# Kernel tuning notes

Measured on AMD Instinct MI355X. Metric: run time of the kernel, lower is better.

Reference implementation:

```python
import jax, jax.numpy as jnp
import numpy as np

B, N, C = 4, 4096, 1024
NUM_HEADS = 16
HEAD_DIM = C // NUM_HEADS


def setup_inputs() -> dict:
    key = jax.random.key(0)
    k1, k2, k3, k4 = jax.random.split(key, 4)
    s_in = 1.0 / np.sqrt(C)
    return {
        "x": jax.random.normal(k1, (B, N, C), dtype=jnp.float32),
        "H": 64,
        "W": 64,
        "Wqkv": jax.random.normal(k2, (3 * C, C), dtype=jnp.float32) * s_in,
        "Wproj": jax.random.normal(k3, (C, C), dtype=jnp.float32) * s_in,
        "bproj": jnp.zeros((C,), dtype=jnp.float32),
        "alpha": jnp.ones((NUM_HEADS,), dtype=jnp.float32),
    }


def reference(x, H, W, Wqkv, Wproj, bproj, alpha):
    Bb, Nn, Cc = x.shape
    h, d = NUM_HEADS, HEAD_DIM
    # qkv: [B, N, 3C] -> [3, B, h, N, d]
    qkv = jnp.einsum('bnc,oc->bno', x, Wqkv)
    qkv = qkv.reshape(Bb, Nn, 3, h, d).transpose(2, 0, 3, 1, 4)
    q, k, v = qkv[0], qkv[1], qkv[2]  # each [B, h, N, d]
    # channel attention: contract over tokens N -> [B, h, d, d]
    attn = jnp.einsum('bhnd,bhne->bhde', k, q) / alpha[None, :, None, None]
    attn = jax.nn.softmax(attn, axis=-1)
    # (dropout is identity in eval/reference mode)
    # head_out: [B, h, d, N] -> transpose -> [B, N, h, d] -> concat heads
    out = jnp.einsum('bhde,bhne->bhdn', attn, v)
    out = out.transpose(0, 3, 1, 2).reshape(Bb, Nn, Cc)
    return jnp.einsum('bnc,oc->bno', out, Wproj) + bproj
```

## Files before the change

kernel.cpp:

```cpp
#include <hip/hip_runtime.h>
#include <hip/hip_bf16.h>
#include <cstdint>
#include <cstddef>

typedef unsigned short u16;
typedef __bf16 bf16x8 __attribute__((ext_vector_type(8)));
typedef float f32x4 __attribute__((ext_vector_type(4)));
typedef unsigned short u16x4 __attribute__((ext_vector_type(4)));
typedef unsigned short u16x8 __attribute__((ext_vector_type(8)));

#define AS1(p) ((__attribute__((address_space(1))) void*)(p))
#define AS3(p) ((__attribute__((address_space(3))) void*)(p))

__device__ __forceinline__ float bf2f(u16 u) {
  unsigned v = ((unsigned)u) << 16; float f; __builtin_memcpy(&f, &v, 4); return f;
}
__device__ __forceinline__ u16 f2bf(float f) {
  unsigned u; __builtin_memcpy(&u, &f, 4);
  u += 0x7FFFu + ((u >> 16) & 1u);
  return (u16)(u >> 16);
}

__global__ __launch_bounds__(256) void convert_kernel(const float* __restrict__ src,
                                                      u16* __restrict__ dst, int n4) {
// ... 54 lines not shown
      llo[(c4 + i) * 72 + rs] = lo[i];
    }
  }
  __syncthreads();
  const int c  = t >> 2;
  const int n0 = (t & 3) * 16;
  const int rot_r = ((t >> 4) & 3) << 4;
  const int nA = n0 ^ rot_r;
  const size_t tbase = ((size_t)b * 1024 + cT * 64 + c) * 4096 + nT * 64 + n0;
  *(u16x8*)(XThi + tbase)     = *(const u16x8*)(lhi + c * 72 + nA);
  *(u16x8*)(XThi + tbase + 8) = *(const u16x8*)(lhi + c * 72 + nA + 8);
  *(u16x8*)(XTlo + tbase)     = *(const u16x8*)(llo + c * 72 + nA);
  *(u16x8*)(XTlo + tbase + 8) = *(const u16x8*)(llo + c * 72 + nA + 8);
}

template<bool OUT_BF16, bool HAS_BIAS>
__global__ __launch_bounds__(512, 2) void gemm_pipe(const u16* __restrict__ A,
                                                    const u16* __restrict__ B,
                                                    void* __restrict__ Cv,
                                                    const float* __restrict__ bias,
                                                    int M, int N, int K,
                                                    size_t sA, size_t sB, size_t sC) {
  __shared__ __align__(16) u16 lds[4][2][8192];
  const int tid  = threadIdx.x;
  const int lane = tid & 63;
  const int wave = tid >> 6;
  const int wm = wave >> 2, wn = wave & 3;
  const int rowTile = blockIdx.x * 256;
  const int colTile = blockIdx.y * 256;
  A += (size_t)blockIdx.z * sA;
  B += (size_t)blockIdx.z * sB;

  size_t srcA[2], srcB[2];
  int ldsOff[2];
#pragma unroll
  for (int j = 0; j < 2; ++j) {
    const int L = j * 512 + tid;
    const int sr = L >> 3;
    const int slot = (L & 7) ^ (sr & 7);
    const int r  = (sr << 1) | (slot >> 2);
    const int kq = slot & 3;
    srcA[j] = (size_t)(rowTile + r) * K + kq * 8;
    srcB[j] = (size_t)(colTile + r) * K + kq * 8;
    ldsOff[j] = (j * 512 + (tid & 448)) * 16;
  }

  const int m15 = lane & 15, kq4 = lane >> 4;
  const int r0a = wm * 128 + m15, sa0 = r0a >> 1;
  const int idxA0 = sa0 * 64 + (((((r0a & 1) << 2) | kq4)) ^ (sa0 & 7)) * 8;
  const int r0b = wn * 64 + m15, sb0 = r0b >> 1;
  const int idxB0 = sb0 * 64 + (((((r0b & 1) << 2) | kq4)) ^ (sb0 & 7)) * 8;

  const int NT = K >> 5;

  auto stageA = [&](int tt) {
    char* d = (char*)&lds[tt & 3][0][0];
    const int kt = tt << 5;
#pragma unroll
    for (int j = 0; j < 2; ++j)
      __builtin_amdgcn_global_load_lds(AS1(A + srcA[j] + kt), AS3(d + ldsOff[j]), 16, 0, 0);
  };
  auto stageB = [&](int tt) {
    char* d = (char*)&lds[tt & 3][1][0];
    const int kt = tt << 5;
#pragma unroll
    for (int j = 0; j < 2; ++j)
      __builtin_amdgcn_global_load_lds(AS1(B + srcB[j] + kt), AS3(d + ldsOff[j]), 16, 0, 0);
  };

  stageA(0); stageB(0);
  if (NT > 1) { stageA(1); stageB(1); }
  if (NT > 2) { stageA(2); stageB(2); }
  if (NT > 2) asm volatile("s_waitcnt vmcnt(8)" ::: "memory");
  else        asm volatile("s_waitcnt vmcnt(0)" ::: "memory");
  __builtin_amdgcn_sched_barrier(0);
  __builtin_amdgcn_s_barrier();
  __builtin_amdgcn_sched_barrier(0);

  f32x4 acc[8][4] = {};
  for (int t = 0; t < NT; ++t) {
    const u16* bufA = &lds[t & 3][0][0];
    const u16* bufB = &lds[t & 3][1][0];
    bf16x8 a[8], bfr[4];
#pragma unroll
    for (int ni = 0; ni < 4; ++ni) bfr[ni] = *(const bf16x8*)(bufB + idxB0 + ni * 512);
#pragma unroll
    for (int mi = 0; mi < 4; ++mi) a[mi] = *(const bf16x8*)(bufA + idxA0 + mi * 512);
    if (t + 3 < NT) stageA(t + 3);
    __builtin_amdgcn_sched_barrier(0);
    __builtin_amdgcn_s_barrier();
    __builtin_amdgcn_sched_barrier(0);
    __builtin_amdgcn_s_setprio(1);
#pragma unroll
    for (int mi = 0; mi < 4; ++mi)
#pragma unroll
      for (int ni = 0; ni < 4; ++ni)
        acc[mi][ni] = __builtin_amdgcn_mfma_f32_16x16x32_bf16(a[mi], bfr[ni], acc[mi][ni], 0, 0, 0);
    __builtin_amdgcn_s_setprio(0);
    __builtin_amdgcn_sched_barrier(0);
    __builtin_amdgcn_s_barrier();
    __builtin_amdgcn_sched_barrier(0);
#pragma unroll
    for (int mi = 4; mi < 8; ++mi) a[mi] = *(const bf16x8*)(bufA + idxA0 + mi * 512);
    if (t + 3 < NT) stageB(t + 3);
    __builtin_amdgcn_sched_barrier(0);
    __builtin_amdgcn_s_barrier();
    __builtin_amdgcn_sched_barrier(0);
    __builtin_amdgcn_s_setprio(1);
#pragma unroll
    for (int mi = 4; mi < 8; ++mi)
#pragma unroll
      for (int ni = 0; ni < 4; ++ni)
        acc[mi][ni] = __builtin_amdgcn_mfma_f32_16x16x32_bf16(a[mi], bfr[ni], acc[mi][ni], 0, 0, 0);
    __builtin_amdgcn_s_setprio(0);
    if (t < NT - 1) {
      if (t + 3 < NT)      asm volatile("s_waitcnt vmcnt(8)" ::: "memory");
      else if (t + 2 < NT) asm volatile("s_waitcnt vmcnt(4)" ::: "memory");
      else                 asm volatile("s_waitcnt vmcnt(0)" ::: "memory");
    }
    __builtin_amdgcn_sched_barrier(0);
    __builtin_amdgcn_s_barrier();
    __builtin_amdgcn_sched_barrier(0);
  }

  const int crow0 = rowTile + wm * 128 + (lane >> 4) * 4;
  const int ccol0 = colTile + wn * 64 + m15;
  if constexpr (OUT_BF16) {
    u16* C = (u16*)Cv + (size_t)blockIdx.z * sC;
#pragma unroll
    for (int mi = 0; mi < 8; ++mi)
#pragma unroll
      for (int ni = 0; ni < 4; ++ni) {
        const int col = ccol0 + ni * 16;
        const float bv = HAS_BIAS ? bias[col] : 0.f;
#pragma unroll
        for (int r = 0; r < 4; ++r)
          C[(size_t)(crow0 + mi * 16 + r) * N + col] = f2bf(acc[mi][ni][r] + bv);
      }
  } else {
    float* C = (float*)Cv + (size_t)blockIdx.z * sC;
#pragma unroll
    for (int mi = 0; mi < 8; ++mi)
#pragma unroll
      for (int ni = 0; ni < 4; ++ni) {
        const int col = ccol0 + ni * 16;
        const float bv = HAS_BIAS ? bias[col] : 0.f;
#pragma unroll
        for (int r = 0; r < 4; ++r)
          C[(size_t)(crow0 + mi * 16 + r) * N + col] = acc[mi][ni][r] + bv;
      }
  }
}

template<int L>
__device__ __forceinline__ void pipe4_core(const u16* __restrict__ pAh,
                                           const u16* __restrict__ pAl,
                                           const u16* __restrict__ pBh,
                                           const u16* __restrict__ pBl,
                                           u16* lds, int ldsByteOff,
                                           int idxA0, int idxB0, int bOff, int NT,
                                           f32x4 acc[4][2]) {
  auto stage2A = [&](int tt) {
    u16* d = lds + (tt & 3) * 16384;
    const int kt = tt << 5;
    __builtin_amdgcn_global_load_lds(AS1(pAh + kt), AS3((char*)d + ldsByteOff), 16, 0, 0);
    __builtin_amdgcn_global_load_lds(AS1(pAl + kt), AS3((char*)(d + 4096) + ldsByteOff), 16, 0, 0);
  };
  auto stage2B = [&](int tt) {
    if constexpr (L == 4) {
      u16* d = lds + (tt & 3) * 16384 + 8192;
      const int kt = tt << 5;
      __builtin_amdgcn_global_load_lds(AS1(pBh + kt), AS3((char*)d + ldsByteOff), 16, 0, 0);
      __builtin_amdgcn_global_load_lds(AS1(pBl + kt), AS3((char*)(d + 4096) + ldsByteOff), 16, 0, 0);
    }
  };

  stage2A(0); stage2B(0);
  stage2A(1); stage2B(1);
  stage2A(2); stage2B(2);
  if constexpr (L == 4) asm volatile("s_waitcnt vmcnt(8)" ::: "memory");
  else                  asm volatile("s_waitcnt vmcnt(4)" ::: "memory");
  __builtin_amdgcn_sched_barrier(0);
  __builtin_amdgcn_s_barrier();
  __builtin_amdgcn_sched_barrier(0);

  for (int t = 0; t < NT; ++t) {
    const u16* base = lds + (t & 3) * 16384;
    bf16x8 ah[4], al[4], bh[2], bl[2];
    bh[0] = *(const bf16x8*)(base + bOff + idxB0);
    bh[1] = *(const bf16x8*)(base + bOff + idxB0 + 512);
    bl[0] = *(const bf16x8*)(base + bOff + 4096 + idxB0);
    bl[1] = *(const bf16x8*)(base + bOff + 4096 + idxB0 + 512);
    ah[0] = *(const bf16x8*)(base + idxA0);
    ah[1] = *(const bf16x8*)(base + idxA0 + 512);
    al[0] = *(const bf16x8*)(base + 4096 + idxA0);
    al[1] = *(const bf16x8*)(base + 4096 + idxA0 + 512);
    if (t + 3 < NT) stage2A(t + 3);
    __builtin_amdgcn_sched_barrier(0);
    __builtin_amdgcn_s_barrier();
    __builtin_amdgcn_sched_barrier(0);
    __builtin_amdgcn_s_setprio(1);
#pragma unroll
    for (int mi = 0; mi < 2; ++mi)
#pragma unroll
      for (int ni = 0; ni < 2; ++ni) {
        acc[mi][ni] = __builtin_amdgcn_mfma_f32_16x16x32_bf16(ah[mi], bh[ni], acc[mi][ni], 0, 0, 0);
        acc[mi][ni] = __builtin_amdgcn_mfma_f32_16x16x32_bf16(ah[mi], bl[ni], acc[mi][ni], 0, 0, 0);
        acc[mi][ni] = __builtin_amdgcn_mfma_f32_16x16x32_bf16(al[mi], bh[ni], acc[mi][ni], 0, 0, 0);
      }
    __builtin_amdgcn_s_setprio(0);
    __builtin_amdgcn_sched_barrier(0);
    __builtin_amdgcn_s_barrier();
    __builtin_amdgcn_sched_barrier(0);
    ah[2] = *(const bf16x8*)(base + idxA0 + 1024);
    ah[3] = *(const bf16x8*)(base + idxA0 + 1536);
    al[2] = *(const bf16x8*)(base + 4096 + idxA0 + 1024);
    al[3] = *(const bf16x8*)(base + 4096 + idxA0 + 1536);
    if (t + 3 < NT) stage2B(t + 3);
    __builtin_amdgcn_sched_barrier(0);
    __builtin_amdgcn_s_barrier();
    __builtin_amdgcn_sched_barrier(0);
    __builtin_amdgcn_s_setprio(1);
#pragma unroll
    for (int mi = 2; mi < 4; ++mi)
#pragma unroll
      for (int ni = 0; ni < 2; ++ni) {
        acc[mi][ni] = __builtin_amdgcn_mfma_f32_16x16x32_bf16(ah[mi], bh[ni], acc[mi][ni], 0, 0, 0);
        acc[mi][ni] = __builtin_amdgcn_mfma_f32_16x16x32_bf16(ah[mi], bl[ni], acc[mi][ni], 0, 0, 0);
        acc[mi][ni] = __builtin_amdgcn_mfma_f32_16x16x32_bf16(al[mi], bh[ni], acc[mi][ni], 0, 0, 0);
      }
    __builtin_amdgcn_s_setprio(0);
    if (t < NT - 1) {
      if constexpr (L == 4) {
        if (t + 3 < NT)      asm volatile("s_waitcnt vmcnt(8)" ::: "memory");
        else if (t + 2 < NT) asm volatile("s_waitcnt vmcnt(4)" ::: "memory");
        else                 asm volatile("s_waitcnt vmcnt(0)" ::: "memory");
      } else {
        if (t + 3 < NT)      asm volatile("s_waitcnt vmcnt(4)" ::: "memory");
        else if (t + 2 < NT) asm volatile("s_waitcnt vmcnt(2)" ::: "memory");
        else                 asm volatile("s_waitcnt vmcnt(0)" ::: "memory");
      }
    }
    __builtin_amdgcn_sched_barrier(0);
    __builtin_amdgcn_s_barrier();
    __builtin_amdgcn_sched_barrier(0);
  }
}

__global__ __launch_bounds__(512, 2) void gram_pipe(const u16* __restrict__ XThi,
                                                    const u16* __restrict__ XTlo,
                                                    float* __restrict__ Gpart) {
  __shared__ __align__(16) u16 lds[4 * 4 * 4096];
  const int tid = threadIdx.x, lane = tid & 63, wave = tid >> 6;
  const int wm = wave >> 2, wn = wave & 3;
  const int bid = blockIdx.x;
  int b, rT, cT, slice, k0, NT; bool same = false;
  if (bid < 64) {
    b = bid & 3; const int j2 = bid >> 2;
    rT = cT = j2 >> 1; slice = j2 & 1; k0 = slice * 2048; NT = 64; same = true;
  } else {
    const int q = bid - 64;
    const int band = q / 112;
    const int e = q % 112;
    b = e & 3; const int pr = e >> 2;
    int t = pr, rt = 0;
    while (t >= 7 - rt) { t -= 7 - rt; ++rt; }
    const int ct = rt + 1 + t;
    constexpr int K0s[4] = {0, 2048, 3584, 3840};
    constexpr int NTs[4] = {64, 48, 8, 8};
    k0 = K0s[band]; NT = NTs[band]; slice = band & 1;
    if (band < 2) { rT = rt; cT = ct; } else { rT = ct; cT = rt; }
  }
  const int rowTile = rT * 128, colTile = cT * 128;
  const u16* Ah = XThi + ((size_t)b << 22);
  const u16* Al = XTlo + ((size_t)b << 22);

  const int sr = tid >> 3;
  const int slot = (tid & 7) ^ (sr & 7);
  const int r = (sr << 1) | (slot >> 2);
  const int kq8 = (slot & 3) * 8;
  const u16* pAh = Ah + (size_t)(rowTile + r) * 4096 + k0 + kq8;
  const u16* pAl = Al + (size_t)(rowTile + r) * 4096 + k0 + kq8;
  const u16* pBh = Ah + (size_t)(colTile + r) * 4096 + k0 + kq8;
  const u16* pBl = Al + (size_t)(colTile + r) * 4096 + k0 + kq8;
  const int ldsByteOff = (tid & 448) * 16;

  const int m15 = lane & 15, kq4 = lane >> 4;
  const int r0a = wm * 64 + m15, sa0 = r0a >> 1;
  const int idxA0 = sa0 * 64 + (((((r0a & 1) << 2) | kq4)) ^ (sa0 & 7)) * 8;
  const int r0b = wn * 32 + m15, sb0 = r0b >> 1;
  const int idxB0 = sb0 * 64 + (((((r0b & 1) << 2) | kq4)) ^ (sb0 & 7)) * 8;

  f32x4 acc[4][2] = {};
  if (same) pipe4_core<2>(pAh, pAl, pAh, pAl, lds, ldsByteOff, idxA0, idxB0, 0, NT, acc);
  else      pipe4_core<4>(pAh, pAl, pBh, pBl, lds, ldsByteOff, idxA0, idxB0, 8192, NT, acc);

  float* out = Gpart + ((size_t)(slice * 4 + b) << 20);
  const int crow0 = rowTile + wm * 64 + (lane >> 4) * 4;
  const int ccol0 = colTile + wn * 32 + m15;
#pragma unroll
  for (int mi = 0; mi < 4; ++mi)
#pragma unroll
    for (int ni = 0; ni < 2; ++ni)
#pragma unroll
      for (int r4 = 0; r4 < 4; ++r4)
        out[(size_t)(crow0 + mi * 16 + r4) * 1024 + ccol0 + ni * 16] = acc[mi][ni][r4];
}

__global__ __launch_bounds__(256) void gram_reduce_split(const float* __restrict__ Gp,
                                                         u16* __restrict__ Ghi,
                                                         u16* __restrict__ Glo) {
  const int rt = blockIdx.x, ct = blockIdx.y, b = blockIdx.z;
  const bool diag128 = (rt >> 1) == (ct >> 1);
  const float* s0 = Gp + ((size_t)b << 20);
  const float* s1 = Gp + ((size_t)(4 + b) << 20);
  __shared__ float lT[64 * 68];
  const int t = threadIdx.x;
  const int r = t >> 2;
  const int c16 = (t & 3) * 16;

  if (!diag128) {
    const size_t bb = (size_t)(ct * 64 + r) * 1024 + rt * 64 + c16;
#pragma unroll
    for (int q = 0; q < 4; ++q) {
      float4 v0 = *(const float4*)(s0 + bb + q * 4);
      float4 v1 = *(const float4*)(s1 + bb + q * 4);
      float4 s = { v0.x + v1.x, v0.y + v1.y, v0.z + v1.z, v0.w + v1.w };
      *(float4*)(lT + r * 68 + c16 + q * 4) = s;
    }
    __syncthreads();
  }

  const size_t ab = (size_t)(rt * 64 + r) * 1024 + ct * 64 + c16;
  const size_t ob = ((size_t)b << 20) + ab;
#pragma unroll
  for (int q = 0; q < 4; ++q) {
    float4 v0 = *(const float4*)(s0 + ab + q * 4);
    float4 v1 = *(const float4*)(s1 + ab + q * 4);
    float g[4] = { v0.x + v1.x, v0.y + v1.y, v0.z + v1.z, v0.w + v1.w };
    if (!diag128) {
#pragma unroll
      for (int i = 0; i < 4; ++i) g[i] += lT[(c16 + q * 4 + i) * 68 + r];
    }
    u16x4 oh, ol;
    oh.x = f2bf(g[0]); ol.x = f2bf(g[0] - bf2f(oh.x));
    oh.y = f2bf(g[1]); ol.y = f2bf(g[1] - bf2f(oh.y));
    oh.z = f2bf(g[2]); ol.z = f2bf(g[2] - bf2f(oh.z));
    oh.w = f2bf(g[3]); ol.w = f2bf(g[3] - bf2f(oh.w));
    *(u16x4*)(Ghi + ob + q * 4) = oh;
    *(u16x4*)(Glo + ob + q * 4) = ol;
  }
}

__global__ __launch_bounds__(512, 2) void tprime_pipe(const u16* __restrict__ Wqh,
                                                      const u16* __restrict__ Wql,
                                                      const u16* __restrict__ Ghi,
                                                      const u16* __restrict__ Glo,
                                                      u16* __restrict__ Tph,
                                                      u16* __restrict__ Tpl) {
  __shared__ __align__(16) u16 lds[4 * 4 * 4096];
  const int tid = threadIdx.x, lane = tid & 63, wave = tid >> 6;
  const int wm = wave >> 2, wn = wave & 3;
  const int bid = blockIdx.x;
  const int b = bid & 3, tile = bid >> 2;
  const int rowTile = (tile >> 3) * 128, colTile = (tile & 7) * 128;
  const size_t zoff = (size_t)b << 20;

  const int sr = tid >> 3;
  const int slot = (tid & 7) ^ (sr & 7);
  const int r = (sr << 1) | (slot >> 2);
  const int kq8 = (slot & 3) * 8;
  const u16* pAh = Wqh + (size_t)(rowTile + r) * 1024 + kq8;
  const u16* pAl = Wql + (size_t)(rowTile + r) * 1024 + kq8;
  const u16* pBh = Ghi + zoff + (size_t)(colTile + r) * 1024 + kq8;
  const u16* pBl = Glo + zoff + (size_t)(colTile + r) * 1024 + kq8;
  const int ldsByteOff = (tid & 448) * 16;

  const int m15 = lane & 15, kq4 = lane >> 4;
  const int r0a = wm * 64 + m15, sa0 = r0a >> 1;
  const int idxA0 = sa0 * 64 + (((((r0a & 1) << 2) | kq4)) ^ (sa0 & 7)) * 8;
  const int r0b = wn * 32 + m15, sb0 = r0b >> 1;
  const int idxB0 = sb0 * 64 + (((((r0b & 1) << 2) | kq4)) ^ (sb0 & 7)) * 8;

  f32x4 acc[4][2] = {};
  pipe4_core<4>(pAh, pAl, pBh, pBl, lds, ldsByteOff, idxA0, idxB0, 8192, 32, acc);

  const int crow0 = rowTile + wm * 64 + (lane >> 4) * 4;
  const int ccol0 = colTile + wn * 32 + m15;
#pragma unroll
  for (int mi = 0; mi < 4; ++mi)
#pragma unroll
    for (int ni = 0; ni < 2; ++ni)
#pragma unroll
      for (int r4 = 0; r4 < 4; ++r4) {
        float v = acc[mi][ni][r4];
        u16 hi = f2bf(v);
        u16 lo = f2bf(v - bf2f(hi));
        size_t off = zoff + (size_t)(crow0 + mi * 16 + r4) * 1024 + ccol0 + ni * 16;
        Tph[off] = hi;
        Tpl[off] = lo;
      }
}

__global__ __launch_bounds__(256) void s_softmax_kernel(const u16* __restrict__ Wqh,
                                                        const u16* __restrict__ Wql,
                                                        const u16* __restrict__ Tph,
                                                        const u16* __restrict__ Tpl,
                                                        const float* __restrict__ alpha,
                                                        u16* __restrict__ attnT) {
  const int h = blockIdx.x, b = blockIdx.y;
  const int tid = threadIdx.x, lane = tid & 63, wave = tid >> 6;
  __shared__ __align__(16) u16 lAh[64 * 32];
  __shared__ __align__(16) u16 lAl[64 * 32];
  __shared__ __align__(16) u16 lBh[64 * 32];
  __shared__ __align__(16) u16 lBl[64 * 32];

  const size_t aBase = (size_t)(1024 + h * 64) * 1024;
  const size_t bBase = ((size_t)b << 20) + (size_t)(h * 64) * 1024;

  f32x4 acc[4] = {};
  const int m  = lane & 15;
  const int ko = (lane >> 4) * 8;
  const int srow = tid >> 2;
  const int skc  = (tid & 3) * 8;
  const int ldsOff = (tid & 192) * 16;

  for (int kt = 0; kt < 1024; kt += 32) {
    __builtin_amdgcn_global_load_lds(AS1(Wqh + aBase + (size_t)srow * 1024 + kt + skc),
                                     AS3((char*)lAh + ldsOff), 16, 0, 0);
    __builtin_amdgcn_global_load_lds(AS1(Wql + aBase + (size_t)srow * 1024 + kt + skc),
                                     AS3((char*)lAl + ldsOff), 16, 0, 0);
    __builtin_amdgcn_global_load_lds(AS1(Tph + bBase + (size_t)srow * 1024 + kt + skc),
                                     AS3((char*)lBh + ldsOff), 16, 0, 0);
    __builtin_amdgcn_global_load_lds(AS1(Tpl + bBase + (size_t)srow * 1024 + kt + skc),
                                     AS3((char*)lBl + ldsOff), 16, 0, 0);
    __syncthreads();
    bf16x8 ah = *(const bf16x8*)(lAh + (wave * 16 + m) * 32 + ko);
    bf16x8 al = *(const bf16x8*)(lAl + (wave * 16 + m) * 32 + ko);
#pragma unroll
    for (int cb = 0; cb < 4; ++cb) {
      bf16x8 bh = *(const bf16x8*)(lBh + (cb * 16 + m) * 32 + ko);
      bf16x8 bl = *(const bf16x8*)(lBl + (cb * 16 + m) * 32 + ko);
      acc[cb] = __builtin_amdgcn_mfma_f32_16x16x32_bf16(ah, bh, acc[cb], 0, 0, 0);
      acc[cb] = __builtin_amdgcn_mfma_f32_16x16x32_bf16(ah, bl, acc[cb], 0, 0, 0);
      acc[cb] = __builtin_amdgcn_mfma_f32_16x16x32_bf16(al, bh, acc[cb], 0, 0, 0);
    }
    __syncthreads();
  }

  const float invA = 1.f / alpha[h];
  const int g = lane >> 4;
  const size_t obase = (size_t)(b * 16 + h) * 4096;
#pragma unroll
  for (int r = 0; r < 4; ++r) {
    int d = wave * 16 + g * 4 + r;
    float s[4];
#pragma unroll
    for (int cb = 0; cb < 4; ++cb) s[cb] = acc[cb][r] * invA;
    float mx = fmaxf(fmaxf(s[0], s[1]), fmaxf(s[2], s[3]));
#pragma unroll
    for (int o = 1; o < 16; o <<= 1) mx = fmaxf(mx, __shfl_xor(mx, o, 64));
    float e[4]; float sum = 0.f;
#pragma unroll
    for (int cb = 0; cb < 4; ++cb) { e[cb] = __expf(s[cb] - mx); sum += e[cb]; }
#pragma unroll
    for (int o = 1; o < 16; o <<= 1) sum += __shfl_xor(sum, o, 64);
    float inv = 1.f / sum;
#pragma unroll
    for (int cb = 0; cb < 4; ++cb) {
      int e_idx = cb * 16 + (lane & 15);
      attnT[obase + (size_t)e_idx * 64 + d] = f2bf(e[cb] * inv);
    }
  }
}

__global__ __launch_bounds__(256) void m_build_kernel(const u16* __restrict__ Wpb,
                                                      const u16* __restrict__ attnT,
                                                      u16* __restrict__ Mb) {
  const int oT = blockIdx.x, h = blockIdx.y, b = blockIdx.z;
  const int tid = threadIdx.x, lane = tid & 63, wave = tid >> 6;
  __shared__ __align__(16) u16 lA[128 * 64];
  __shared__ __align__(16) u16 lB[64 * 64];
  const int bh = b * 16 + h;
#pragma unroll
  for (int i = 0; i < 4; ++i) {
    int idx = i * 256 + tid;
    int row = idx >> 3;
    int kc  = (idx & 7) * 8;
    int ldsOff = (i * 256 + (tid & 192)) * 16;
    __builtin_amdgcn_global_load_lds(AS1(Wpb + (size_t)(oT * 128 + row) * 1024 + h * 64 + kc),
                                     AS3((char*)lA + ldsOff), 16, 0, 0);
  }
#pragma unroll
  for (int i = 0; i < 2; ++i) {
    int idx = i * 256 + tid;
    int ldsOff = (i * 256 + (tid & 192)) * 16;
    __builtin_amdgcn_global_load_lds(AS1(attnT + (size_t)bh * 4096 + idx * 8),
                                     AS3((char*)lB + ldsOff), 16, 0, 0);
  }
  __syncthreads();
  const int m  = lane & 15;
  const int ko = (lane >> 4) * 8;
  const int wr = wave * 32;
  f32x4 acc[2][4] = {};
#pragma unroll
  for (int ks = 0; ks < 2; ++ks) {
#pragma unroll
    for (int rb = 0; rb < 2; ++rb) {
      bf16x8 a = *(const bf16x8*)(lA + (wr + rb * 16 + m) * 64 + ks * 32 + ko);
#pragma unroll
      for (int cb = 0; cb < 4; ++cb) {
        bf16x8 bb = *(const bf16x8*)(lB + (cb * 16 + m) * 64 + ks * 32 + ko);
        acc[rb][cb] = __builtin_amdgcn_mfma_f32_16x16x32_bf16(a, bb, acc[rb][cb], 0, 0, 0);
      }
    }
  }
  u16* out = Mb + ((size_t)b << 20);
#pragma unroll
  for (int rb = 0; rb < 2; ++rb)
#pragma unroll
    for (int cb = 0; cb < 4; ++cb) {
      int col = h * 64 + cb * 16 + (lane & 15);
#pragma unroll
      for (int r = 0; r < 4; ++r) {
        int row = oT * 128 + wr + rb * 16 + (lane >> 4) * 4 + r;
        out[(size_t)row * 1024 + col] = f2bf(acc[rb][cb][r]);
      }
    }
}

extern "C" void kernel_launch(void* const* d_in, const int* in_sizes, int n_in,
                              void* d_out, int out_size, void* d_ws, size_t ws_size,
                              hipStream_t stream) {
  const float* x     = (const float*)d_in[0];
  const float* Wqkv  = (const float*)d_in[3];
  const float* Wproj = (const float*)d_in[4];
  const float* bproj = (const float*)d_in[5];
  const float* alpha = (const float*)d_in[6];

  char* ws = (char*)d_ws;
  u16*   Xb     = (u16*)ws;
  float* Gpart  = (float*)ws;
  u16*   Mb     = (u16*)ws;
  u16*   XThi   = (u16*)(ws + 33554432);
  u16*   attnTb = (u16*)(ws + 33554432);
  u16*   XTlo  = (u16*)(ws + 67108864);
  u16*   Ghi   = (u16*)(ws + 67108864);
  u16*   Glo   = (u16*)(ws + 75497472);
  u16*   Tph   = (u16*)(ws + 83886080);
  u16*   Tpl   = (u16*)(ws + 92274688);
  u16*   Wqh   = (u16*)(ws + 100663296);
  u16*   Wql   = (u16*)(ws + 106954752);
  u16*   Vb    = (u16*)(ws + 113246208);
  u16*   Wpb   = (u16*)(ws + 146800640);

  transpose_split_kernel<<<dim3(64, 16, 4), 256, 0, stream>>>(x, Xb, XThi, XTlo);
  convert_split_kernel<<<256, 256, 0, stream>>>(Wqkv, Wqh, Wql, 3145728 / 4);
  convert_kernel<<<128, 256, 0, stream>>>(Wproj, Wpb, 1048576 / 4);
  gemm_pipe<true, false><<<dim3(64, 4, 1), 512, 0, stream>>>(
      Xb, Wqh + (size_t)2048 * 1024, Vb, nullptr, 16384, 1024, 1024,
      (size_t)0, (size_t)0, (size_t)0);
  gram_pipe<<<dim3(512), 512, 0, stream>>>(XThi, XTlo, Gpart);
  gram_reduce_split<<<dim3(16, 16, 4), 256, 0, stream>>>(Gpart, Ghi, Glo);
  tprime_pipe<<<dim3(256), 512, 0, stream>>>(Wqh, Wql, Ghi, Glo, Tph, Tpl);
  s_softmax_kernel<<<dim3(16, 4), 256, 0, stream>>>(Wqh, Wql, Tph, Tpl, alpha, attnTb);
  m_build_kernel<<<dim3(8, 16, 4), 256, 0, stream>>>(Wpb, attnTb, Mb);
  gemm_pipe<false, true><<<dim3(16, 4, 4), 512, 0, stream>>>(
      Vb, Mb, (float*)d_out, bproj, 4096, 1024, 1024,
      (size_t)1 << 22, (size_t)1 << 20, (size_t)1 << 22);
}
```

Measured before the change: 382.5 us.

## Split K across wave halves with 64x64 warp tiles and LDS reduction in gram/tprime

Reworks the shared GEMM pipeline so the 8 waves form two groups of four. Each group processes alternate K tiles (intra-block split-K) with larger 64x64 per-wave output tiles, then the two halves' accumulators are summed through LDS before the store. Loads are now staged two K-tiles at a time. The gram kernel's work partition also changes from uneven K bands to four equal 1024-wide K quarters. The aim is more MFMA work per LDS fragment read and a more balanced grid. In exchange it needs more accumulator registers per wave and adds an LDS reduction step.

Result: no change. 381.9 us (-0.2%).

```diff
diff --git a/kernel.cpp b/kernel.cpp
--- a/kernel.cpp
+++ b/kernel.cpp
@@ -231,49 +231,45 @@
 }
 
 template<int L>
-__device__ __forceinline__ void pipe4_core(const u16* __restrict__ pAh,
-                                           const u16* __restrict__ pAl,
-                                           const u16* __restrict__ pBh,
-                                           const u16* __restrict__ pBl,
-                                           u16* lds, int ldsByteOff,
-                                           int idxA0, int idxB0, int bOff, int NT,
-                                           f32x4 acc[4][2]) {
-  auto stage2A = [&](int tt) {
+__device__ __forceinline__ void pipe4k_core(const u16* __restrict__ pAh,
+                                            const u16* __restrict__ pAl,
+                                            const u16* __restrict__ pBh,
+                                            const u16* __restrict__ pBl,
+                                            u16* lds, int ldsByteOff,
+                                            int idxA0, int idxB0, int bOff,
+                                            int NT, int half,
+                                            f32x4 acc[4][4]) {
+  auto stage = [&](int tt) {
     u16* d = lds + (tt & 3) * 16384;
     const int kt = tt << 5;
     __builtin_amdgcn_global_load_lds(AS1(pAh + kt), AS3((char*)d + ldsByteOff), 16, 0, 0);
     __builtin_amdgcn_global_load_lds(AS1(pAl + kt), AS3((char*)(d + 4096) + ldsByteOff), 16, 0, 0);
+    if constexpr (L == 4) {
+      __builtin_amdgcn_global_load_lds(AS1(pBh + kt), AS3((char*)(d + 8192) + ldsByteOff), 16, 0, 0);
+      __builtin_amdgcn_global_load_lds(AS1(pBl + kt), AS3((char*)(d + 12288) + ldsByteOff), 16, 0, 0);
+    }
   };
-  auto stage2B = [&](int tt) {
-    if constexpr (L == 4) {
-      u16* d = lds + (tt & 3) * 16384 + 8192;
-      const int kt = tt << 5;
-      __builtin_amdgcn_global_load_lds(AS1(pBh + kt), AS3((char*)d + ldsByteOff), 16, 0, 0);
-      __builtin_amdgcn_global_load_lds(AS1(pBl + kt), AS3((char*)(d + 4096) + ldsByteOff), 16, 0, 0);
-    }
-  };
-
-  stage2A(0); stage2B(0);
-  stage2A(1); stage2B(1);
-  stage2A(2); stage2B(2);
+
+  stage(0); stage(1); stage(2); stage(3);
   if constexpr (L == 4) asm volatile("s_waitcnt vmcnt(8)" ::: "memory");
   else                  asm volatile("s_waitcnt vmcnt(4)" ::: "memory");
   __builtin_amdgcn_sched_barrier(0);
   __builtin_amdgcn_s_barrier();
   __builtin_amdgcn_sched_barrier(0);
 
-  for (int t = 0; t < NT; ++t) {
-    const u16* base = lds + (t & 3) * 16384;
-    bf16x8 ah[4], al[4], bh[2], bl[2];
-    bh[0] = *(const bf16x8*)(base + bOff + idxB0);
-    bh[1] = *(const bf16x8*)(base + bOff + idxB0 + 512);
-    bl[0] = *(const bf16x8*)(base + bOff + 4096 + idxB0);
-    bl[1] = *(const bf16x8*)(base + bOff + 4096 + idxB0 + 512);
+  const int npairs = NT >> 1;
+  for (int i = 0; i < npairs; ++i) {
+    const u16* base = lds + ((2 * i + half) & 3) * 16384;
+    bf16x8 ah[4], al[4], bh[4], bl[4];
+#pragma unroll
+    for (int ni = 0; ni < 4; ++ni) {
+      bh[ni] = *(const bf16x8*)(base + bOff + idxB0 + ni * 512);
+      bl[ni] = *(const bf16x8*)(base + bOff + 4096 + idxB0 + ni * 512);
+    }
     ah[0] = *(const bf16x8*)(base + idxA0);
     ah[1] = *(const bf16x8*)(base + idxA0 + 512);
     al[0] = *(const bf16x8*)(base + 4096 + idxA0);
     al[1] = *(const bf16x8*)(base + 4096 + idxA0 + 512);
-    if (t + 3 < NT) stage2A(t + 3);
     __builtin_amdgcn_sched_barrier(0);
     __builtin_amdgcn_s_barrier();
     __builtin_amdgcn_sched_barrier(0);
@@ -281,7 +277,7 @@
 #pragma unroll
     for (int mi = 0; mi < 2; ++mi)
 #pragma unroll
-      for (int ni = 0; ni < 2; ++ni) {
+      for (int ni = 0; ni < 4; ++ni) {
         acc[mi][ni] = __builtin_amdgcn_mfma_f32_16x16x32_bf16(ah[mi], bh[ni], acc[mi][ni], 0, 0, 0);
         acc[mi][ni] = __builtin_amdgcn_mfma_f32_16x16x32_bf16(ah[mi], bl[ni], acc[mi][ni], 0, 0, 0);
         acc[mi][ni] = __builtin_amdgcn_mfma_f32_16x16x32_bf16(al[mi], bh[ni], acc[mi][ni], 0, 0, 0);
@@ -294,29 +290,27 @@
     ah[3] = *(const bf16x8*)(base + idxA0 + 1536);
     al[2] = *(const bf16x8*)(base + 4096 + idxA0 + 1024);
     al[3] = *(const bf16x8*)(base + 4096 + idxA0 + 1536);
-    if (t + 3 < NT) stage2B(t + 3);
-    __builtin_amdgcn_sched_barrier(0);
-    __builtin_amdgcn_s_barrier();
+    __builtin_amdgcn_sched_barrier(0);
+    __builtin_amdgcn_s_barrier();
+    __builtin_amdgcn_sched_barrier(0);
+    if (i + 2 < npairs) { stage(2 * i + 4); stage(2 * i + 5); }
     __builtin_amdgcn_sched_barrier(0);
     __builtin_amdgcn_s_setprio(1);
 #pragma unroll
     for (int mi = 2; mi < 4; ++mi)
 #pragma unroll
-      for (int ni = 0; ni < 2; ++ni) {
+      for (int ni = 0; ni < 4; ++ni) {
         acc[mi][ni] = __builtin_amdgcn_mfma_f32_16x16x32_bf16(ah[mi], bh[ni], acc[mi][ni], 0, 0, 0);
         acc[mi][ni] = __builtin_amdgcn_mfma_f32_16x16x32_bf16(ah[mi], bl[ni], acc[mi][ni], 0, 0, 0);
         acc[mi][ni] = __builtin_amdgcn_mfma_f32_16x16x32_bf16(al[mi], bh[ni], acc[mi][ni], 0, 0, 0);
       }
     __builtin_amdgcn_s_setprio(0);
-    if (t < NT - 1) {
-      if constexpr (L == 4) {
-        if (t + 3 < NT)      asm volatile("s_waitcnt vmcnt(8)" ::: "memory");
-        else if (t + 2 < NT) asm volatile("s_waitcnt vmcnt(4)" ::: "memory");
-        else                 asm volatile("s_waitcnt vmcnt(0)" ::: "memory");
+    if (i < npairs - 1) {
+      if (i + 2 < npairs) {
+        if constexpr (L == 4) asm volatile("s_waitcnt vmcnt(8)" ::: "memory");
+        else                  asm volatile("s_waitcnt vmcnt(4)" ::: "memory");
       } else {
-        if (t + 3 < NT)      asm volatile("s_waitcnt vmcnt(4)" ::: "memory");
-        else if (t + 2 < NT) asm volatile("s_waitcnt vmcnt(2)" ::: "memory");
-        else                 asm volatile("s_waitcnt vmcnt(0)" ::: "memory");
+        asm volatile("s_waitcnt vmcnt(0)" ::: "memory");
       }
     }
     __builtin_amdgcn_sched_barrier(0);
@@ -328,26 +322,24 @@
 __global__ __launch_bounds__(512, 2) void gram_pipe(const u16* __restrict__ XThi,
                                                     const u16* __restrict__ XTlo,
                                                     float* __restrict__ Gpart) {
-  __shared__ __align__(16) u16 lds[4 * 4 * 4096];
+  __shared__ __align__(16) u16 ldsmem[4 * 4 * 4096];
   const int tid = threadIdx.x, lane = tid & 63, wave = tid >> 6;
-  const int wm = wave >> 2, wn = wave & 3;
+  const int q = wave & 3, half = wave >> 2;
+  const int qm = q >> 1, qn = q & 1;
   const int bid = blockIdx.x;
   int b, rT, cT, slice, k0, NT; bool same = false;
   if (bid < 64) {
     b = bid & 3; const int j2 = bid >> 2;
     rT = cT = j2 >> 1; slice = j2 & 1; k0 = slice * 2048; NT = 64; same = true;
   } else {
-    const int q = bid - 64;
-    const int band = q / 112;
-    const int e = q % 112;
-    b = e & 3; const int pr = e >> 2;
-    int t = pr, rt = 0;
+    const int e = bid - 64; b = e & 3;
+    const int idx = e >> 2; const int tile = idx >> 2, kq = idx & 3;
+    int t = tile, rt = 0;
     while (t >= 7 - rt) { t -= 7 - rt; ++rt; }
     const int ct = rt + 1 + t;
-    constexpr int K0s[4] = {0, 2048, 3584, 3840};
-    constexpr int NTs[4] = {64, 48, 8, 8};
-    k0 = K0s[band]; NT = NTs[band]; slice = band & 1;
-    if (band < 2) { rT = rt; cT = ct; } else { rT = ct; cT = rt; }
+    rT = rt; cT = ct;
+    if (kq >= 2) { rT = ct; cT = rt; }
+    slice = kq & 1; k0 = kq * 1024; NT = 32;
   }
   const int rowTile = rT * 128, colTile = cT * 128;
   const u16* Ah = XThi + ((size_t)b << 22);
@@ -364,25 +356,40 @@
   const int ldsByteOff = (tid & 448) * 16;
 
   const int m15 = lane & 15, kq4 = lane >> 4;
-  const int r0a = wm * 64 + m15, sa0 = r0a >> 1;
+  const int r0a = qm * 64 + m15, sa0 = r0a >> 1;
   const int idxA0 = sa0 * 64 + (((((r0a & 1) << 2) | kq4)) ^ (sa0 & 7)) * 8;
-  const int r0b = wn * 32 + m15, sb0 = r0b >> 1;
+  const int r0b = qn * 64 + m15, sb0 = r0b >> 1;
   const int idxB0 = sb0 * 64 + (((((r0b & 1) << 2) | kq4)) ^ (sb0 & 7)) * 8;
 
-  f32x4 acc[4][2] = {};
-  if (same) pipe4_core<2>(pAh, pAl, pAh, pAl, lds, ldsByteOff, idxA0, idxB0, 0, NT, acc);
-  else      pipe4_core<4>(pAh, pAl, pBh, pBl, lds, ldsByteOff, idxA0, idxB0, 8192, NT, acc);
-
-  float* out = Gpart + ((size_t)(slice * 4 + b) << 20);
-  const int crow0 = rowTile + wm * 64 + (lane >> 4) * 4;
-  const int ccol0 = colTile + wn * 32 + m15;
-#pragma unroll
-  for (int mi = 0; mi < 4; ++mi)
-#pragma unroll
-    for (int ni = 0; ni < 2; ++ni)
-#pragma unroll
-      for (int r4 = 0; r4 < 4; ++r4)
-        out[(size_t)(crow0 + mi * 16 + r4) * 1024 + ccol0 + ni * 16] = acc[mi][ni][r4];
+  f32x4 acc[4][4] = {};
+  if (same) pipe4k_core<2>(pAh, pAl, pAh, pAl, ldsmem, ldsByteOff, idxA0, idxB0, 0, NT, half, acc);
+  else      pipe4k_core<4>(pAh, pAl, pBh, pBl, ldsmem, ldsByteOff, idxA0, idxB0, 8192, NT, half, acc);
+
+  float* red = (float*)ldsmem;
+  const int rr = (lane >> 4) * 4;
+  if (half) {
+#pragma unroll
+    for (int mi = 0; mi < 4; ++mi)
+#pragma unroll
+      for (int ni = 0; ni < 4; ++ni)
+        *(f32x4*)(red + q * 4352 + (ni * 16 + m15) * 68 + mi * 16 + rr) = acc[mi][ni];
+  }
+  __syncthreads();
+  if (!half) {
+    float* out = Gpart + ((size_t)(slice * 4 + b) << 20);
+    const int crow0 = rowTile + qm * 64 + rr;
+    const int ccol0 = colTile + qn * 64 + m15;
+#pragma unroll
+    for (int mi = 0; mi < 4; ++mi)
+#pragma unroll
+      for (int ni = 0; ni < 4; ++ni) {
+        f32x4 v = *(const f32x4*)(red + q * 4352 + (ni * 16 + m15) * 68 + mi * 16 + rr);
+        v += acc[mi][ni];
+#pragma unroll
+        for (int r4 = 0; r4 < 4; ++r4)
+          out[(size_t)(crow0 + mi * 16 + r4) * 1024 + ccol0 + ni * 16] = v[r4];
+      }
+  }
 }
 
 __global__ __launch_bounds__(256) void gram_reduce_split(const float* __restrict__ Gp,
@@ -436,9 +443,10 @@
                                                       const u16* __restrict__ Glo,
                                                       u16* __restrict__ Tph,
                                                       u16* __restrict__ Tpl) {
-  __shared__ __align__(16) u16 lds[4 * 4 * 4096];
+  __shared__ __align__(16) u16 ldsmem[4 * 4 * 4096];
   const int tid = threadIdx.x, lane = tid & 63, wave = tid >> 6;
-  const int wm = wave >> 2, wn = wave & 3;
+  const int q = wave & 3, half = wave >> 2;
+  const int qm = q >> 1, qn = q & 1;
   const int bid = blockIdx.x;
   const int b = bid & 3, tile = bid >> 2;
   const int rowTile = (tile >> 3) * 128, colTile = (tile & 7) * 128;
@@ -455,29 +463,44 @@
   const int ldsByteOff = (tid & 448) * 16;
 
   const int m15 = lane & 15, kq4 = lane >> 4;
-  const int r0a = wm * 64 + m15, sa0 = r0a >> 1;
+  const int r0a = qm * 64 + m15, sa0 = r0a >> 1;
   const int idxA0 = sa0 * 64 + (((((r0a & 1) << 2) | kq4)) ^ (sa0 & 7)) * 8;
-  const int r0b = wn * 32 + m15, sb0 = r0b >> 1;
+  const int r0b = qn * 64 + m15, sb0 = r0b >> 1;
   const int idxB0 = sb0 * 64 + (((((r0b & 1) << 2) | kq4)) ^ (sb0 & 7)) * 8;
 
-  f32x4 acc[4][2] = {};
-  pipe4_core<4>(pAh, pAl, pBh, pBl, lds, ldsByteOff, idxA0, idxB0, 8192, 32, acc);
-
-  const int crow0 = rowTile + wm * 64 + (lane >> 4) * 4;
-  const int ccol0 = colTile + wn * 32 + m15;
-#pragma unroll
-  for (int mi = 0; mi < 4; ++mi)
-#pragma unroll
-    for (int ni = 0; ni < 2; ++ni)
-#pragma unroll
-      for (int r4 = 0; r4 < 4; ++r4) {
-        float v = acc[mi][ni][r4];
-        u16 hi = f2bf(v);
-        u16 lo = f2bf(v - bf2f(hi));
-        size_t off = zoff + (size_t)(crow0 + mi * 16 + r4) * 1024 + ccol0 + ni * 16;
-        Tph[off] = hi;
-        Tpl[off] = lo;
-      }
+  f32x4 acc[4][4] = {};
+  pipe4k_core<4>(pAh, pAl, pBh, pBl, ldsmem, ldsByteOff, idxA0, idxB0, 8192, 32, half, acc);
+
+  float* red = (float*)ldsmem;
+  const int rr = (lane >> 4) * 4;
+  if (half) {
+#pragma unroll
+    for (int mi = 0; mi < 4; ++mi)
+#pragma unroll
+      for (int ni = 0; ni < 4; ++ni)
+        *(f32x4*)(red + q * 4352 + (ni * 16 + m15) * 68 + mi * 16 + rr) = acc[mi][ni];
+  }
+  __syncthreads();
+  if (!half) {
+    const int crow0 = rowTile + qm * 64 + rr;
+    const int ccol0 = colTile + qn * 64 + m15;
+#pragma unroll
+    for (int mi = 0; mi < 4; ++mi)
+#pragma unroll
+      for (int ni = 0; ni < 4; ++ni) {
+        f32x4 v = *(const f32x4*)(red + q * 4352 + (ni * 16 + m15) * 68 + mi * 16 + rr);
+        v += acc[mi][ni];
+#pragma unroll
+        for (int r4 = 0; r4 < 4; ++r4) {
+          float x = v[r4];
+          u16 hi = f2bf(x);
+          u16 lo = f2bf(x - bf2f(hi));
+          size_t off = zoff + (size_t)(crow0 + mi * 16 + r4) * 1024 + ccol0 + ni * 16;
+          Tph[off] = hi;
+          Tpl[off] = lo;
+        }
+      }
+  }
 }
 
 __global__ __launch_bounds__(256) void s_softmax_kernel(const u16* __restrict__ Wqh,
```

## Replace symmetric split-K Gram and reduce with segmented full-tile pipelined GEMM

Applied to the files above, without the earlier changes.

Replaces the triangular split-K Gram kernel plus its fp32 partial reduction with a generic kernel that computes every 128x128 tile of the full Gram matrix, running the three hi/lo product terms as concatenated K segments in one pipeline. The same kernel is reused for the T' product, and the workspace layout is compacted. This removes the fp32 partial write/read and one launch, at the cost of recomputing the symmetric half of the Gram matrix with only 256 blocks and longer K loops.

After: 675.9 us. 1.77x slower.

```diff
diff --git a/kernel.cpp b/kernel.cpp
--- a/kernel.cpp
+++ b/kernel.cpp
@@ -230,138 +230,32 @@
   }
 }
 
-template<int L>
-__device__ __forceinline__ void pipe4_core(const u16* __restrict__ pAh,
-                                           const u16* __restrict__ pAl,
-                                           const u16* __restrict__ pBh,
-                                           const u16* __restrict__ pBl,
-                                           u16* lds, int ldsByteOff,
-                                           int idxA0, int idxB0, int bOff, int NT,
-                                           f32x4 acc[4][2]) {
-  auto stage2A = [&](int tt) {
-    u16* d = lds + (tt & 3) * 16384;
-    const int kt = tt << 5;
-    __builtin_amdgcn_global_load_lds(AS1(pAh + kt), AS3((char*)d + ldsByteOff), 16, 0, 0);
-    __builtin_amdgcn_global_load_lds(AS1(pAl + kt), AS3((char*)(d + 4096) + ldsByteOff), 16, 0, 0);
-  };
-  auto stage2B = [&](int tt) {
-    if constexpr (L == 4) {
-      u16* d = lds + (tt & 3) * 16384 + 8192;
-      const int kt = tt << 5;
-      __builtin_amdgcn_global_load_lds(AS1(pBh + kt), AS3((char*)d + ldsByteOff), 16, 0, 0);
-      __builtin_amdgcn_global_load_lds(AS1(pBl + kt), AS3((char*)(d + 4096) + ldsByteOff), 16, 0, 0);
-    }
-  };
-
-  stage2A(0); stage2B(0);
-  stage2A(1); stage2B(1);
-  stage2A(2); stage2B(2);
-  if constexpr (L == 4) asm volatile("s_waitcnt vmcnt(8)" ::: "memory");
-  else                  asm volatile("s_waitcnt vmcnt(4)" ::: "memory");
-  __builtin_amdgcn_sched_barrier(0);
-  __builtin_amdgcn_s_barrier();
-  __builtin_amdgcn_sched_barrier(0);
-
-  for (int t = 0; t < NT; ++t) {
-    const u16* base = lds + (t & 3) * 16384;
-    bf16x8 ah[4], al[4], bh[2], bl[2];
-    bh[0] = *(const bf16x8*)(base + bOff + idxB0);
-    bh[1] = *(const bf16x8*)(base + bOff + idxB0 + 512);
-    bl[0] = *(const bf16x8*)(base + bOff + 4096 + idxB0);
-    bl[1] = *(const bf16x8*)(base + bOff + 4096 + idxB0 + 512);
-    ah[0] = *(const bf16x8*)(base + idxA0);
-    ah[1] = *(const bf16x8*)(base + idxA0 + 512);
-    al[0] = *(const bf16x8*)(base + 4096 + idxA0);
-    al[1] = *(const bf16x8*)(base + 4096 + idxA0 + 512);
-    if (t + 3 < NT) stage2A(t + 3);
-    __builtin_amdgcn_sched_barrier(0);
-    __builtin_amdgcn_s_barrier();
-    __builtin_amdgcn_sched_barrier(0);
-    __builtin_amdgcn_s_setprio(1);
-#pragma unroll
-    for (int mi = 0; mi < 2; ++mi)
-#pragma unroll
-      for (int ni = 0; ni < 2; ++ni) {
-        acc[mi][ni] = __builtin_amdgcn_mfma_f32_16x16x32_bf16(ah[mi], bh[ni], acc[mi][ni], 0, 0, 0);
-        acc[mi][ni] = __builtin_amdgcn_mfma_f32_16x16x32_bf16(ah[mi], bl[ni], acc[mi][ni], 0, 0, 0);
-        acc[mi][ni] = __builtin_amdgcn_mfma_f32_16x16x32_bf16(al[mi], bh[ni], acc[mi][ni], 0, 0, 0);
-      }
-    __builtin_amdgcn_s_setprio(0);
-    __builtin_amdgcn_sched_barrier(0);
-    __builtin_amdgcn_s_barrier();
-    __builtin_amdgcn_sched_barrier(0);
-    ah[2] = *(const bf16x8*)(base + idxA0 + 1024);
-    ah[3] = *(const bf16x8*)(base + idxA0 + 1536);
-    al[2] = *(const bf16x8*)(base + 4096 + idxA0 + 1024);
-    al[3] = *(const bf16x8*)(base + 4096 + idxA0 + 1536);
-    if (t + 3 < NT) stage2B(t + 3);
-    __builtin_amdgcn_sched_barrier(0);
-    __builtin_amdgcn_s_barrier();
-    __builtin_amdgcn_sched_barrier(0);
-    __builtin_amdgcn_s_setprio(1);
-#pragma unroll
-    for (int mi = 2; mi < 4; ++mi)
-#pragma unroll
-      for (int ni = 0; ni < 2; ++ni) {
-        acc[mi][ni] = __builtin_amdgcn_mfma_f32_16x16x32_bf16(ah[mi], bh[ni], acc[mi][ni], 0, 0, 0);
-        acc[mi][ni] = __builtin_amdgcn_mfma_f32_16x16x32_bf16(ah[mi], bl[ni], acc[mi][ni], 0, 0, 0);
-        acc[mi][ni] = __builtin_amdgcn_mfma_f32_16x16x32_bf16(al[mi], bh[ni], acc[mi][ni], 0, 0, 0);
-      }
-    __builtin_amdgcn_s_setprio(0);
-    if (t < NT - 1) {
-      if constexpr (L == 4) {
-        if (t + 3 < NT)      asm volatile("s_waitcnt vmcnt(8)" ::: "memory");
-        else if (t + 2 < NT) asm volatile("s_waitcnt vmcnt(4)" ::: "memory");
-        else                 asm volatile("s_waitcnt vmcnt(0)" ::: "memory");
-      } else {
-        if (t + 3 < NT)      asm volatile("s_waitcnt vmcnt(4)" ::: "memory");
-        else if (t + 2 < NT) asm volatile("s_waitcnt vmcnt(2)" ::: "memory");
-        else                 asm volatile("s_waitcnt vmcnt(0)" ::: "memory");
-      }
-    }
-    __builtin_amdgcn_sched_barrier(0);
-    __builtin_amdgcn_s_barrier();
-    __builtin_amdgcn_sched_barrier(0);
-  }
-}
-
-__global__ __launch_bounds__(512, 2) void gram_pipe(const u16* __restrict__ XThi,
-                                                    const u16* __restrict__ XTlo,
-                                                    float* __restrict__ Gpart) {
-  __shared__ __align__(16) u16 lds[4 * 4 * 4096];
+template<int LOGSEG>
+__global__ __launch_bounds__(512, 2) void pipe2_seg(const u16* __restrict__ A0,
+                                                    const u16* __restrict__ A1,
+                                                    const u16* __restrict__ A2,
+                                                    const u16* __restrict__ B0,
+                                                    const u16* __restrict__ B1,
+                                                    const u16* __restrict__ B2,
+                                                    u16* __restrict__ Ohi,
+                                                    u16* __restrict__ Olo,
+                                                    int ldA, int ldB, int NT,
+                                                    size_t sA, size_t sB, size_t sO) {
+  __shared__ __align__(16) u16 lds[4 * 8192];
   const int tid = threadIdx.x, lane = tid & 63, wave = tid >> 6;
   const int wm = wave >> 2, wn = wave & 3;
-  const int bid = blockIdx.x;
-  int b, rT, cT, slice, k0, NT; bool same = false;
-  if (bid < 64) {
-    b = bid & 3; const int j2 = bid >> 2;
-    rT = cT = j2 >> 1; slice = j2 & 1; k0 = slice * 2048; NT = 64; same = true;
-  } else {
-    const int q = bid - 64;
-    const int band = q / 112;
-    const int e = q % 112;
-    b = e & 3; const int pr = e >> 2;
-    int t = pr, rt = 0;
-    while (t >= 7 - rt) { t -= 7 - rt; ++rt; }
-    const int ct = rt + 1 + t;
-    constexpr int K0s[4] = {0, 2048, 3584, 3840};
-    constexpr int NTs[4] = {64, 48, 8, 8};
-    k0 = K0s[band]; NT = NTs[band]; slice = band & 1;
-    if (band < 2) { rT = rt; cT = ct; } else { rT = ct; cT = rt; }
-  }
-  const int rowTile = rT * 128, colTile = cT * 128;
-  const u16* Ah = XThi + ((size_t)b << 22);
-  const u16* Al = XTlo + ((size_t)b << 22);
+  const int b = blockIdx.x & 3, tile = blockIdx.x >> 2;
+  const int rowTile = (tile >> 3) * 128, colTile = (tile & 7) * 128;
 
   const int sr = tid >> 3;
   const int slot = (tid & 7) ^ (sr & 7);
   const int r = (sr << 1) | (slot >> 2);
   const int kq8 = (slot & 3) * 8;
-  const u16* pAh = Ah + (size_t)(rowTile + r) * 4096 + k0 + kq8;
-  const u16* pAl = Al + (size_t)(rowTile + r) * 4096 + k0 + kq8;
-  const u16* pBh = Ah + (size_t)(colTile + r) * 4096 + k0 + kq8;
-  const u16* pBl = Al + (size_t)(colTile + r) * 4096 + k0 + kq8;
-  const int ldsByteOff = (tid & 448) * 16;
+  const size_t aRow = (size_t)(rowTile + r) * ldA + kq8 + b * sA;
+  const size_t bRow = (size_t)(colTile + r) * ldB + kq8 + b * sB;
+  const u16* pA0 = A0 + aRow; const u16* pA1 = A1 + aRow; const u16* pA2 = A2 + aRow;
+  const u16* pB0 = B0 + bRow; const u16* pB1 = B1 + bRow; const u16* pB2 = B2 + bRow;
+  const int off = (tid & 448) * 16;
 
   const int m15 = lane & 15, kq4 = lane >> 4;
   const int r0a = wm * 64 + m15, sa0 = r0a >> 1;
@@ -369,100 +263,63 @@
   const int r0b = wn * 32 + m15, sb0 = r0b >> 1;
   const int idxB0 = sb0 * 64 + (((((r0b & 1) << 2) | kq4)) ^ (sb0 & 7)) * 8;
 
+  auto stage = [&](int tt) {
+    u16* d = lds + (tt & 3) * 8192;
+    const int seg = tt >> LOGSEG;
+    const int kk = (tt & ((1 << LOGSEG) - 1)) << 5;
+    const u16* pa = (seg == 0) ? pA0 : ((seg == 1) ? pA1 : pA2);
+    const u16* pb = (seg == 0) ? pB0 : ((seg == 1) ? pB1 : pB2);
+    __builtin_amdgcn_global_load_lds(AS1(pa + kk), AS3((char*)d + off), 16, 0, 0);
+    __builtin_amdgcn_global_load_lds(AS1(pb + kk), AS3((char*)(d + 4096) + off), 16, 0, 0);
+  };
+
+  stage(0); stage(1); stage(2); stage(3);
+  asm volatile("s_waitcnt vmcnt(4)" ::: "memory");
+  __builtin_amdgcn_sched_barrier(0);
+  __builtin_amdgcn_s_barrier();
+  __builtin_amdgcn_sched_barrier(0);
+
   f32x4 acc[4][2] = {};
-  if (same) pipe4_core<2>(pAh, pAl, pAh, pAl, lds, ldsByteOff, idxA0, idxB0, 0, NT, acc);
-  else      pipe4_core<4>(pAh, pAl, pBh, pBl, lds, ldsByteOff, idxA0, idxB0, 8192, NT, acc);
-
-  float* out = Gpart + ((size_t)(slice * 4 + b) << 20);
-  const int crow0 = rowTile + wm * 64 + (lane >> 4) * 4;
-  const int ccol0 = colTile + wn * 32 + m15;
-#pragma unroll
-  for (int mi = 0; mi < 4; ++mi)
-#pragma unroll
-    for (int ni = 0; ni < 2; ++ni)
-#pragma unroll
-      for (int r4 = 0; r4 < 4; ++r4)
-        out[(size_t)(crow0 + mi * 16 + r4) * 1024 + ccol0 + ni * 16] = acc[mi][ni][r4];
-}
-
-__global__ __launch_bounds__(256) void gram_reduce_split(const float* __restrict__ Gp,
-                                                         u16* __restrict__ Ghi,
-                                                         u16* __restrict__ Glo) {
-  const int rt = blockIdx.x, ct = blockIdx.y, b = blockIdx.z;
-  const bool diag128 = (rt >> 1) == (ct >> 1);
-  const float* s0 = Gp + ((size_t)b << 20);
-  const float* s1 = Gp + ((size_t)(4 + b) << 20);
-  __shared__ float lT[64 * 68];
-  const int t = threadIdx.x;
-  const int r = t >> 2;
-  const int c16 = (t & 3) * 16;
-
-  if (!diag128) {
-    const size_t bb = (size_t)(ct * 64 + r) * 1024 + rt * 64 + c16;
-#pragma unroll
-    for (int q = 0; q < 4; ++q) {
-      float4 v0 = *(const float4*)(s0 + bb + q * 4);
-      float4 v1 = *(const float4*)(s1 + bb + q * 4);
-      float4 s = { v0.x + v1.x, v0.y + v1.y, v0.z + v1.z, v0.w + v1.w };
-      *(float4*)(lT + r * 68 + c16 + q * 4) = s;
-    }
-    __syncthreads();
-  }
-
-  const size_t ab = (size_t)(rt * 64 + r) * 1024 + ct * 64 + c16;
-  const size_t ob = ((size_t)b << 20) + ab;
-#pragma unroll
-  for (int q = 0; q < 4; ++q) {
-    float4 v0 = *(const float4*)(s0 + ab + q * 4);
-    float4 v1 = *(const float4*)(s1 + ab + q * 4);
-    float g[4] = { v0.x + v1.x, v0.y + v1.y, v0.z + v1.z, v0.w + v1.w };
-    if (!diag128) {
-#pragma unroll
-      for (int i = 0; i < 4; ++i) g[i] += lT[(c16 + q * 4 + i) * 68 + r];
-    }
-    u16x4 oh, ol;
-    oh.x = f2bf(g[0]); ol.x = f2bf(g[0] - bf2f(oh.x));
-    oh.y = f2bf(g[1]); ol.y = f2bf(g[1] - bf2f(oh.y));
-    oh.z = f2bf(g[2]); ol.z = f2bf(g[2] - bf2f(oh.z));
-    oh.w = f2bf(g[3]); ol.w = f2bf(g[3] - bf2f(oh.w));
-    *(u16x4*)(Ghi + ob + q * 4) = oh;
-    *(u16x4*)(Glo + ob + q * 4) = ol;
-  }
-}
-
-__global__ __launch_bounds__(512, 2) void tprime_pipe(const u16* __restrict__ Wqh,
-                                                      const u16* __restrict__ Wql,
-                                                      const u16* __restrict__ Ghi,
-                                                      const u16* __restrict__ Glo,
-                                                      u16* __restrict__ Tph,
-                                                      u16* __restrict__ Tpl) {
-  __shared__ __align__(16) u16 lds[4 * 4 * 4096];
-  const int tid = threadIdx.x, lane = tid & 63, wave = tid >> 6;
-  const int wm = wave >> 2, wn = wave & 3;
-  const int bid = blockIdx.x;
-  const int b = bid & 3, tile = bid >> 2;
-  const int rowTile = (tile >> 3) * 128, colTile = (tile & 7) * 128;
-  const size_t zoff = (size_t)b << 20;
-
-  const int sr = tid >> 3;
-  const int slot = (tid & 7) ^ (sr & 7);
-  const int r = (sr << 1) | (slot >> 2);
-  const int kq8 = (slot & 3) * 8;
-  const u16* pAh = Wqh + (size_t)(rowTile + r) * 1024 + kq8;
-  const u16* pAl = Wql + (size_t)(rowTile + r) * 1024 + kq8;
-  const u16* pBh = Ghi + zoff + (size_t)(colTile + r) * 1024 + kq8;
-  const u16* pBl = Glo + zoff + (size_t)(colTile + r) * 1024 + kq8;
-  const int ldsByteOff = (tid & 448) * 16;
-
-  const int m15 = lane & 15, kq4 = lane >> 4;
-  const int r0a = wm * 64 + m15, sa0 = r0a >> 1;
-  const int idxA0 = sa0 * 64 + (((((r0a & 1) << 2) | kq4)) ^ (sa0 & 7)) * 8;
-  const int r0b = wn * 32 + m15, sb0 = r0b >> 1;
-  const int idxB0 = sb0 * 64 + (((((r0b & 1) << 2) | kq4)) ^ (sb0 & 7)) * 8;
-
-  f32x4 acc[4][2] = {};
-  pipe4_core<4>(pAh, pAl, pBh, pBl, lds, ldsByteOff, idxA0, idxB0, 8192, 32, acc);
-
+  const int npairs = NT >> 1;
+  for (int i = 0; i < npairs; ++i) {
+    const u16* e0 = lds + ((2 * i) & 3) * 8192;
+    const u16* e1 = lds + ((2 * i + 1) & 3) * 8192;
+    bf16x8 a0[4], a1[4], f0[2], f1[2];
+#pragma unroll
+    for (int mi = 0; mi < 4; ++mi) {
+      a0[mi] = *(const bf16x8*)(e0 + idxA0 + mi * 512);
+      a1[mi] = *(const bf16x8*)(e1 + idxA0 + mi * 512);
+    }
+#pragma unroll
+    for (int ni = 0; ni < 2; ++ni) {
+      f0[ni] = *(const bf16x8*)(e0 + 4096 + idxB0 + ni * 512);
+      f1[ni] = *(const bf16x8*)(e1 + 4096 + idxB0 + ni * 512);
+    }
+    __builtin_amdgcn_sched_barrier(0);
+    __builtin_amdgcn_s_barrier();
+    __builtin_amdgcn_sched_barrier(0);
+    if (i + 2 < npairs) { stage(2 * i + 4); stage(2 * i + 5); }
+    __builtin_amdgcn_sched_barrier(0);
+    __builtin_amdgcn_s_setprio(1);
+#pragma unroll
+    for (int mi = 0; mi < 4; ++mi)
+#pragma unroll
+      for (int ni = 0; ni < 2; ++ni) {
+        acc[mi][ni] = __builtin_amdgcn_mfma_f32_16x16x32_bf16(a0[mi], f0[ni], acc[mi][ni], 0, 0, 0);
+        acc[mi][ni] = __builtin_amdgcn_mfma_f32_16x16x32_bf16(a1[mi], f1[ni], acc[mi][ni], 0, 0, 0);
+      }
+    __builtin_amdgcn_s_setprio(0);
+    if (i < npairs - 1) {
+      if (i + 2 < npairs) asm volatile("s_waitcnt vmcnt(4)" ::: "memory");
+      else                asm volatile("s_waitcnt vmcnt(0)" ::: "memory");
+    }
+    __builtin_amdgcn_sched_barrier(0);
+    __builtin_amdgcn_s_barrier();
+    __builtin_amdgcn_sched_barrier(0);
+  }
+
+  u16* oh = Ohi + b * sO;
+  u16* ol = Olo + b * sO;
   const int crow0 = rowTile + wm * 64 + (lane >> 4) * 4;
   const int ccol0 = colTile + wn * 32 + m15;
 #pragma unroll
@@ -474,9 +331,9 @@
         float v = acc[mi][ni][r4];
         u16 hi = f2bf(v);
         u16 lo = f2bf(v - bf2f(hi));
-        size_t off = zoff + (size_t)(crow0 + mi * 16 + r4) * 1024 + ccol0 + ni * 16;
-        Tph[off] = hi;
-        Tpl[off] = lo;
+        size_t o = (size_t)(crow0 + mi * 16 + r4) * 1024 + ccol0 + ni * 16;
+        oh[o] = hi;
+        ol[o] = lo;
       }
 }
 
@@ -617,20 +474,19 @@
   const float* alpha = (const float*)d_in[6];
 
   char* ws = (char*)d_ws;
-  u16*   Xb     = (u16*)ws;
-  float* Gpart  = (float*)ws;
-  u16*   Mb     = (u16*)ws;
+  u16*   Xb   = (u16*)ws;
+  u16*   Ghi  = (u16*)ws;
+  u16*   Glo  = (u16*)(ws + 8388608);
+  u16*   Tph  = (u16*)(ws + 16777216);
+  u16*   Tpl  = (u16*)(ws + 25165824);
+  u16*   Mb   = (u16*)(ws + 16777216);
   u16*   XThi   = (u16*)(ws + 33554432);
   u16*   attnTb = (u16*)(ws + 33554432);
-  u16*   XTlo  = (u16*)(ws + 67108864);
-  u16*   Ghi   = (u16*)(ws + 67108864);
-  u16*   Glo   = (u16*)(ws + 75497472);
-  u16*   Tph   = (u16*)(ws + 83886080);
-  u16*   Tpl   = (u16*)(ws + 92274688);
-  u16*   Wqh   = (u16*)(ws + 100663296);
-  u16*   Wql   = (u16*)(ws + 106954752);
-  u16*   Vb    = (u16*)(ws + 113246208);
-  u16*   Wpb   = (u16*)(ws + 146800640);
+  u16*   XTlo = (u16*)(ws + 67108864);
+  u16*   Wqh  = (u16*)(ws + 100663296);
+  u16*   Wql  = (u16*)(ws + 106954752);
+  u16*   Vb   = (u16*)(ws + 113246208);
+  u16*   Wpb  = (u16*)(ws + 146800640);
 
   transpose_split_kernel<<<dim3(64, 16, 4), 256, 0, stream>>>(x, Xb, XThi, XTlo);
   convert_split_kernel<<<256, 256, 0, stream>>>(Wqkv, Wqh, Wql, 3145728 / 4);
@@ -638,9 +494,12 @@
   gemm_pipe<true, false><<<dim3(64, 4, 1), 512, 0, stream>>>(
       Xb, Wqh + (size_t)2048 * 1024, Vb, nullptr, 16384, 1024, 1024,
       (size_t)0, (size_t)0, (size_t)0);
-  gram_pipe<<<dim3(512), 512, 0, stream>>>(XThi, XTlo, Gpart);
-  gram_reduce_split<<<dim3(16, 16, 4), 256, 0, stream>>>(Gpart, Ghi, Glo);
-  tprime_pipe<<<dim3(256), 512, 0, stream>>>(Wqh, Wql, Ghi, Glo, Tph, Tpl);
+  pipe2_seg<7><<<dim3(256), 512, 0, stream>>>(
+      XThi, XTlo, XThi, XThi, XThi, XTlo, Ghi, Glo,
+      4096, 4096, 384, (size_t)1 << 22, (size_t)1 << 22, (size_t)1 << 20);
+  pipe2_seg<5><<<dim3(256), 512, 0, stream>>>(
+      Wqh, Wql, Wqh, Ghi, Ghi, Glo, Tph, Tpl,
+      1024, 1024, 96, (size_t)0, (size_t)1 << 20, (size_t)1 << 20);
   s_softmax_kernel<<<dim3(16, 4), 256, 0, stream>>>(Wqh, Wql, Tph, Tpl, alpha, attnTb);
   m_build_kernel<<<dim3(8, 16, 4), 256, 0, stream>>>(Wpb, attnTb, Mb);
   gemm_pipe<false, true><<<dim3(16, 4, 4), 512, 0, stream>>>(
```
